# Kernel optimization log

Hardware: AMD Instinct MI355X
Metric: run time of the kernel (lower is better)

The kernel has to match this reference:

```python
import jax, jax.numpy as jnp
import numpy as np

POOLED = 7      # kernel_size
SCALE = 0.25    # spatial_scale
GMAX = 2        # upper bound of adaptive sampling grid (box sizes chosen so ceil(roi/7) <= 2)


def setup_inputs() -> dict:
    key = jax.random.key(0)
    k1, k2, k3, k4, k5, k6 = jax.random.split(key, 6)
    B, C, H, W, K = 4, 256, 128, 128, 1000
    features = jax.random.normal(k1, (B, C, H, W), dtype=jnp.float32)
    img = H / SCALE  # 512.0: image-space extent
    bidx = jax.random.randint(k2, (K,), 0, B).astype(jnp.float32)
    bw = jax.random.uniform(k3, (K,), minval=8.0, maxval=56.0)
    bh = jax.random.uniform(k4, (K,), minval=8.0, maxval=56.0)
    x1 = jax.random.uniform(k5, (K,), minval=0.0, maxval=img - 56.0)
    y1 = jax.random.uniform(k6, (K,), minval=0.0, maxval=img - 56.0)
    boxes = jnp.stack([bidx, x1, y1, x1 + bw, y1 + bh], axis=1)
    return {"features": features, "boxes": boxes}


def _sample_coords(start, bin_sz, grid):
    # start/bin_sz/grid: [K] -> coords [K, POOLED, GMAX]
    p = jnp.arange(POOLED, dtype=jnp.float32)
    i = jnp.arange(GMAX, dtype=jnp.float32)
    return (start[:, None, None] + p[None, :, None] * bin_sz[:, None, None]
            + (i[None, None, :] + 0.5) * bin_sz[:, None, None] / grid[:, None, None])


def roi_align(features, boxes):
    B, C, H, W = features.shape
    K = boxes.shape[0]
    b = boxes[:, 0].astype(jnp.int32)
    x1, y1, x2, y2 = (boxes[:, i] * SCALE for i in (1, 2, 3, 4))
    # aligned=False: no -0.5 offset, clamp roi size to >= 1
    roi_w = jnp.maximum(x2 - x1, 1.0)
    roi_h = jnp.maximum(y2 - y1, 1.0)
    bin_w = roi_w / POOLED
    bin_h = roi_h / POOLED
    # sampling_ratio = -1 -> adaptive grid = ceil(roi_size / pooled)
    gh = jnp.ceil(roi_h / POOLED)
    gw = jnp.ceil(roi_w / POOLED)

    y = _sample_coords(y1, bin_h, gh)  # [K,7,GMAX]
    x = _sample_coords(x1, bin_w, gw)  # [K,7,GMAX]
    vy = (jnp.arange(GMAX)[None, None, :] < gh[:, None, None])  # [K,1,GMAX]
    vx = (jnp.arange(GMAX)[None, None, :] < gw[:, None, None])

    # full sample grid [K, 7, GMAX, 7, GMAX] -> flatten to [K, P]
    shp = (K, POOLED, GMAX, POOLED, GMAX)
    Y = jnp.broadcast_to(y[:, :, :, None, None], shp).reshape(K, -1)
    X = jnp.broadcast_to(x[:, None, None, :, :], shp).reshape(K, -1)
    V = jnp.broadcast_to(vy[:, :, :, None, None] & vx[:, None, None, :, :], shp).reshape(K, -1)

    # bilinear interpolation, torchvision boundary semantics
    inval = (Y < -1.0) | (Y > H) | (X < -1.0) | (X > W)
    Yc = jnp.clip(Y, 0.0)
    Xc = jnp.clip(X, 0.0)
    yl = jnp.minimum(Yc.astype(jnp.int32), H - 1)
    xl = jnp.minimum(Xc.astype(jnp.int32), W - 1)
    yh = jnp.minimum(yl + 1, H - 1)
    xh = jnp.minimum(xl + 1, W - 1)
    Yc = jnp.where(yl >= H - 1, yl.astype(jnp.float32), Yc)
    Xc = jnp.where(xl >= W - 1, xl.astype(jnp.float32), Xc)
    ly = Yc - yl
    lx = Xc - xl
    hy = 1.0 - ly
    hx = 1.0 - lx
    m = jnp.where(inval | (~V), 0.0, 1.0)
    w1 = hy * hx * m; w2 = hy * lx * m; w3 = ly * hx * m; w4 = ly * lx * m

    def gather(yi, xi):
        # advanced indexing: [K,P] indices -> [K,P,C]
        return features[b[:, None], :, yi, xi]

    val = (w1[..., None] * gather(yl, xl) + w2[..., None] * gather(yl, xh)
           + w3[..., None] * gather(yh, xl) + w4[..., None] * gather(yh, xh))  # [K,P,C]
    val = val.reshape(K, POOLED, GMAX, POOLED, GMAX, C)
    out = val.sum(axis=(2, 4)) / (gh * gw)[:, None, None, None]  # [K,7,7,C]
    return jnp.transpose(out, (0, 3, 1, 2))  # [K,C,7,7]


def reference(features, boxes):
    return roi_align(features, boxes)
```

## Files before the change

### kernel.cpp

```cpp
#include <hip/hip_runtime.h>

#define POOLED 7
#define SCALE  0.25f
#define CCH    256
#define HH     128
#define WW     128
#define HW     (HH * WW)

#define NCH      16
#define NCHUNK   2
#define NBLK_PER_BOX (CCH / (NCH * NCHUNK))
#define PATCH_H  15
#define PATCH_W  16
#define PIXROW   17
#define NPIX     (14 * PIXROW + 16)
#define CHPAD    20

__global__ __launch_bounds__(256) void roi_align_kernel(
    const float* __restrict__ feat,
    const float* __restrict__ boxes,
    float* __restrict__ out,
    int K)
{
    __shared__ float patch[NPIX * CHPAD];

    int bx = blockIdx.x;
    int k  = bx >> 3;
    int cb = (bx & 7) * (NCH * NCHUNK);
    if (k >= K) return;
    int t = threadIdx.x;

    const float* box = boxes + (size_t)k * 5;
    int   b  = (int)box[0];
    float x1 = box[1] * SCALE;
    float y1 = box[2] * SCALE;
    float x2 = box[3] * SCALE;
    float y2 = box[4] * SCALE;

    float roi_w = fmaxf(x2 - x1, 1.0f);
    float roi_h = fmaxf(y2 - y1, 1.0f);
    float bin_w = roi_w * (1.0f / POOLED);
    float bin_h = roi_h * (1.0f / POOLED);
    int gw = (int)ceilf(roi_w * (1.0f / POOLED));
    int gh = (int)ceilf(roi_h * (1.0f / POOLED));
    float inv_gh = 1.0f / (float)gh;
    float inv_gw = 1.0f / (float)gw;
    int ns = gh * gw;

    float ymin = y1 + 0.5f * bin_h * inv_gh;
    float ymax = y1 + 6 * bin_h + ((gh - 1) + 0.5f) * bin_h * inv_gh;
    float xmin = x1 + 0.5f * bin_w * inv_gw;

    int ylo = min((int)fmaxf(ymin, 0.0f), HH - 1);
    int xlo = min((int)fmaxf(xmin, 0.0f), WW - 1);
    int ylmax = min((int)fmaxf(ymax, 0.0f), HH - 1);
    int h_p = min(ylmax + 1, HH - 1) - ylo + 1;
    if (h_p > PATCH_H) h_p = PATCH_H;

    int p  = t & 63;
    int pc = min(p, 48);
    int pw = pc % POOLED;
    int ph = pc / POOLED;
    int c4 = t >> 6;

    float wa[4], wb[4], wc_[4], wd[4];
    int   oa[4], ob[4], oc[4], od[4];

#pragma unroll
    for (int s = 0; s < 4; ++s) {
        if (s >= ns) break;
        int iy = s % gh;
        int ix = s / gh;

        float y = y1 + ph * bin_h + (iy + 0.5f) * bin_h * inv_gh;
        float x = x1 + pw * bin_w + (ix + 0.5f) * bin_w * inv_gw;
        bool valid = (y >= -1.0f) && (y <= (float)HH) && (x >= -1.0f) && (x <= (float)WW);

        float yc = fmaxf(y, 0.0f);
        int yl = min((int)yc, HH - 1);
        int yh2 = min(yl + 1, HH - 1);
        float ly = (yl >= HH - 1) ? 0.0f : (yc - (float)yl);
        float hy = 1.0f - ly;

        float xc = fmaxf(x, 0.0f);
        int xl = min((int)xc, WW - 1);
        int xh2 = min(xl + 1, WW - 1);
        float lx = (xl >= WW - 1) ? 0.0f : (xc - (float)xl);
        float hx = 1.0f - lx;

        float m = valid ? 1.0f : 0.0f;
        wa[s]  = hy * hx * m;
        wb[s]  = hy * lx * m;
        wc_[s] = ly * hx * m;
        wd[s]  = ly * lx * m;

        int ry  = max(0, min(yl  - ylo, h_p - 1));
        int ryh = max(0, min(yh2 - ylo, h_p - 1));
        int rxl = max(0, min(xl  - xlo, PATCH_W - 1));
        int rxh = max(0, min(xh2 - xlo, PATCH_W - 1));
        oa[s] = (ry  * PIXROW + rxl) * CHPAD;
        ob[s] = (ry  * PIXROW + rxh) * CHPAD;
        oc[s] = (ryh * PIXROW + rxl) * CHPAD;
        od[s] = (ryh * PIXROW + rxh) * CHPAD;
    }

    int lch  = t >> 4;
    int lcol = t & 15;
    int xcol = min(xlo + lcol, WW - 1);
    float sc = inv_gh * inv_gw;

    for (int ch = 0; ch < NCHUNK; ++ch) {
        if (ch) __syncthreads();

        {
            const float* g = feat + ((size_t)b * CCH + cb + ch * NCH + lch) * HW + xcol;
            float* lp = patch + lcol * CHPAD + lch;
            for (int r = 0; r < h_p; ++r) {
                lp[r * (PIXROW * CHPAD)] = g[(ylo + r) * WW];
            }
        }
        __syncthreads();

        if (p < 49) {
            float4 acc = {0.0f, 0.0f, 0.0f, 0.0f};
            const float* cp = patch + c4 * 4;
#pragma unroll
            for (int s = 0; s < 4; ++s) {
                if (s >= ns) break;
                float4 va = *(const float4*)(cp + oa[s]);
                float4 vb = *(const float4*)(cp + ob[s]);
                float4 vc = *(const float4*)(cp + oc[s]);
                float4 vd = *(const float4*)(cp + od[s]);
                float w1 = wa[s], w2 = wb[s], w3 = wc_[s], w4 = wd[s];
                acc.x += w1 * va.x + w2 * vb.x + w3 * vc.x + w4 * vd.x;
                acc.y += w1 * va.y + w2 * vb.y + w3 * vc.y + w4 * vd.y;
                acc.z += w1 * va.z + w2 * vb.z + w3 * vc.z + w4 * vd.z;
                acc.w += w1 * va.w + w2 * vb.w + w3 * vc.w + w4 * vd.w;
            }
            float* obase = out + ((size_t)k * CCH + cb + ch * NCH + c4 * 4) * 49 + p;
            obase[0]      = acc.x * sc;
            obase[49]     = acc.y * sc;
            obase[2 * 49] = acc.z * sc;
            obase[3 * 49] = acc.w * sc;
        }
    }
}

extern "C" void kernel_launch(void* const* d_in, const int* in_sizes, int n_in,
                              void* d_out, int out_size, void* d_ws, size_t ws_size,
                              hipStream_t stream) {
    const float* feat  = (const float*)d_in[0];
    const float* boxes = (const float*)d_in[1];
    float* out = (float*)d_out;

    int K = in_sizes[1] / 5;
    int blocks = K * NBLK_PER_BOX;
    roi_align_kernel<<<blocks, 256, 0, stream>>>(feat, boxes, out, K);
}
```

Baseline: 133.0 us.

## Vectorize patch loads with float4 and prefetch second channel chunk into registers

The patch load now reads float4 vectors from a 4-aligned column start, widening the patch to 20 columns, instead of scalar per-column loads in a row loop. The second channel chunk's global loads are issued before the first chunk is computed, so global latency overlaps with the LDS compute of chunk one. Sample index math swaps div/mod for shift/mask, which assumes gh is 1 or 2. This raises register use and LDS size, and the alignment clamp near the right edge needs care.

```diff
diff --git a/kernel.cpp b/kernel.cpp
--- a/kernel.cpp
+++ b/kernel.cpp
@@ -11,9 +11,10 @@
 #define NCHUNK   2
 #define NBLK_PER_BOX (CCH / (NCH * NCHUNK))
 #define PATCH_H  15
-#define PATCH_W  16
-#define PIXROW   17
-#define NPIX     (14 * PIXROW + 16)
+#define PATCH_W  20
+#define NV       5
+#define PIXROW   21
+#define NPIX     (14 * PIXROW + PATCH_W)
 #define CHPAD    20
 
 __global__ __launch_bounds__(256) void roi_align_kernel(
@@ -22,7 +23,7 @@
     float* __restrict__ out,
     int K)
 {
-    __shared__ float patch[NPIX * CHPAD];
+    __shared__ __align__(16) float patch[NPIX * CHPAD];
 
     int bx = blockIdx.x;
     int k  = bx >> 3;
@@ -53,15 +54,18 @@
 
     int ylo = min((int)fmaxf(ymin, 0.0f), HH - 1);
     int xlo = min((int)fmaxf(xmin, 0.0f), WW - 1);
+    int xlo4 = xlo & ~3;
     int ylmax = min((int)fmaxf(ymax, 0.0f), HH - 1);
     int h_p = min(ylmax + 1, HH - 1) - ylo + 1;
     if (h_p > PATCH_H) h_p = PATCH_H;
+    int mcr = min(WW - 1 - xlo4, (xlo - xlo4) + 15);
 
     int p  = t & 63;
     int pc = min(p, 48);
     int pw = pc % POOLED;
     int ph = pc / POOLED;
     int c4 = t >> 6;
+    int ghm = gh - 1;
 
     float wa[4], wb[4], wc_[4], wd[4];
     int   oa[4], ob[4], oc[4], od[4];
@@ -69,8 +73,8 @@
 #pragma unroll
     for (int s = 0; s < 4; ++s) {
         if (s >= ns) break;
-        int iy = s % gh;
-        int ix = s / gh;
+        int iy = s & ghm;
+        int ix = s >> ghm;
 
         float y = y1 + ph * bin_h + (iy + 0.5f) * bin_h * inv_gh;
         float x = x1 + pw * bin_w + (ix + 0.5f) * bin_w * inv_gw;
@@ -96,53 +100,113 @@
 
         int ry  = max(0, min(yl  - ylo, h_p - 1));
         int ryh = max(0, min(yh2 - ylo, h_p - 1));
-        int rxl = max(0, min(xl  - xlo, PATCH_W - 1));
-        int rxh = max(0, min(xh2 - xlo, PATCH_W - 1));
+        int rxl = max(0, min(xl  - xlo4, PATCH_W - 1));
+        int rxh = max(0, min(xh2 - xlo4, PATCH_W - 1));
         oa[s] = (ry  * PIXROW + rxl) * CHPAD;
         ob[s] = (ry  * PIXROW + rxh) * CHPAD;
         oc[s] = (ryh * PIXROW + rxl) * CHPAD;
         od[s] = (ryh * PIXROW + rxh) * CHPAD;
     }
 
-    int lch  = t >> 4;
-    int lcol = t & 15;
-    int xcol = min(xlo + lcol, WW - 1);
+    int lch = t >> 4;
+    int sub = t & 15;
+    int lim = h_p * NV;
+    const float* gch0 = feat + ((size_t)b * CCH + cb + lch) * HW;
+
+    bool act[NV];
+    int  goff[NV];
+    int  la[NV];
+#pragma unroll
+    for (int i = 0; i < NV; ++i) {
+        int idx = i * 16 + sub;
+        int r = idx / NV;
+        int v = idx - r * NV;
+        act[i]  = (idx < lim) && (4 * v <= mcr);
+        goff[i] = (ylo + r) * WW + min(xlo4 + 4 * v, WW - 4);
+        la[i]   = (r * PIXROW + 4 * v) * CHPAD + lch;
+    }
+
     float sc = inv_gh * inv_gw;
 
-    for (int ch = 0; ch < NCHUNK; ++ch) {
-        if (ch) __syncthreads();
-
-        {
-            const float* g = feat + ((size_t)b * CCH + cb + ch * NCH + lch) * HW + xcol;
-            float* lp = patch + lcol * CHPAD + lch;
-            for (int r = 0; r < h_p; ++r) {
-                lp[r * (PIXROW * CHPAD)] = g[(ylo + r) * WW];
-            }
-        }
-        __syncthreads();
-
-        if (p < 49) {
-            float4 acc = {0.0f, 0.0f, 0.0f, 0.0f};
-            const float* cp = patch + c4 * 4;
-#pragma unroll
-            for (int s = 0; s < 4; ++s) {
-                if (s >= ns) break;
-                float4 va = *(const float4*)(cp + oa[s]);
-                float4 vb = *(const float4*)(cp + ob[s]);
-                float4 vc = *(const float4*)(cp + oc[s]);
-                float4 vd = *(const float4*)(cp + od[s]);
-                float w1 = wa[s], w2 = wb[s], w3 = wc_[s], w4 = wd[s];
-                acc.x += w1 * va.x + w2 * vb.x + w3 * vc.x + w4 * vd.x;
-                acc.y += w1 * va.y + w2 * vb.y + w3 * vc.y + w4 * vd.y;
-                acc.z += w1 * va.z + w2 * vb.z + w3 * vc.z + w4 * vd.z;
-                acc.w += w1 * va.w + w2 * vb.w + w3 * vc.w + w4 * vd.w;
-            }
-            float* obase = out + ((size_t)k * CCH + cb + ch * NCH + c4 * 4) * 49 + p;
-            obase[0]      = acc.x * sc;
-            obase[49]     = acc.y * sc;
-            obase[2 * 49] = acc.z * sc;
-            obase[3 * 49] = acc.w * sc;
-        }
+    float4 v0[NV];
+#pragma unroll
+    for (int i = 0; i < NV; ++i)
+        if (act[i]) v0[i] = *(const float4*)(gch0 + goff[i]);
+#pragma unroll
+    for (int i = 0; i < NV; ++i)
+        if (act[i]) {
+            float* lp = patch + la[i];
+            lp[0]         = v0[i].x;
+            lp[CHPAD]     = v0[i].y;
+            lp[2 * CHPAD] = v0[i].z;
+            lp[3 * CHPAD] = v0[i].w;
+        }
+
+    const float* gch1 = gch0 + (size_t)NCH * HW;
+    float4 v1[NV];
+#pragma unroll
+    for (int i = 0; i < NV; ++i)
+        if (act[i]) v1[i] = *(const float4*)(gch1 + goff[i]);
+
+    __syncthreads();
+
+    if (p < 49) {
+        float4 acc = {0.0f, 0.0f, 0.0f, 0.0f};
+        const float* cp = patch + c4 * 4;
+#pragma unroll
+        for (int s = 0; s < 4; ++s) {
+            if (s >= ns) break;
+            float4 va = *(const float4*)(cp + oa[s]);
+            float4 vb = *(const float4*)(cp + ob[s]);
+            float4 vc = *(const float4*)(cp + oc[s]);
+            float4 vd = *(const float4*)(cp + od[s]);
+            float w1 = wa[s], w2 = wb[s], w3 = wc_[s], w4 = wd[s];
+            acc.x += w1 * va.x + w2 * vb.x + w3 * vc.x + w4 * vd.x;
+            acc.y += w1 * va.y + w2 * vb.y + w3 * vc.y + w4 * vd.y;
+            acc.z += w1 * va.z + w2 * vb.z + w3 * vc.z + w4 * vd.z;
+            acc.w += w1 * va.w + w2 * vb.w + w3 * vc.w + w4 * vd.w;
+        }
+        float* obase = out + ((size_t)k * CCH + cb + c4 * 4) * 49 + p;
+        obase[0]      = acc.x * sc;
+        obase[49]     = acc.y * sc;
+        obase[2 * 49] = acc.z * sc;
+        obase[3 * 49] = acc.w * sc;
+    }
+
+    __syncthreads();
+
+#pragma unroll
+    for (int i = 0; i < NV; ++i)
+        if (act[i]) {
+            float* lp = patch + la[i];
+            lp[0]         = v1[i].x;
+            lp[CHPAD]     = v1[i].y;
+            lp[2 * CHPAD] = v1[i].z;
+            lp[3 * CHPAD] = v1[i].w;
+        }
+    __syncthreads();
+
+    if (p < 49) {
+        float4 acc = {0.0f, 0.0f, 0.0f, 0.0f};
+        const float* cp = patch + c4 * 4;
+#pragma unroll
+        for (int s = 0; s < 4; ++s) {
+            if (s >= ns) break;
+            float4 va = *(const float4*)(cp + oa[s]);
+            float4 vb = *(const float4*)(cp + ob[s]);
+            float4 vc = *(const float4*)(cp + oc[s]);
+            float4 vd = *(const float4*)(cp + od[s]);
+            float w1 = wa[s], w2 = wb[s], w3 = wc_[s], w4 = wd[s];
+            acc.x += w1 * va.x + w2 * vb.x + w3 * vc.x + w4 * vd.x;
+            acc.y += w1 * va.y + w2 * vb.y + w3 * vc.y + w4 * vd.y;
+            acc.z += w1 * va.z + w2 * vb.z + w3 * vc.z + w4 * vd.z;
+            acc.w += w1 * va.w + w2 * vb.w + w3 * vc.w + w4 * vd.w;
+        }
+        float* obase = out + ((size_t)k * CCH + cb + NCH + c4 * 4) * 49 + p;
+        obase[0]      = acc.x * sc;
+        obase[49]     = acc.y * sc;
+        obase[2 * 49] = acc.z * sc;
+        obase[3 * 49] = acc.w * sc;
     }
 }
 
```

New measurement: 127.2 us. -4.3%, faster.

## Vectorize patch loads as float4 and prefetch second channel chunk

Applied to the files above, without the earlier changes.

Patch loading switches from one scalar global load per row per thread to aligned float4 loads over a 4-aligned column window. The window is widened to 19 columns so each row is covered by five vector loads. The second channel chunk is issued into registers before the first chunk is computed, which overlaps its global latency with the first bilinear pass. Sample weights are built from separable per-axis terms with uniform scalars, and launch bounds ask for 7 blocks per CU. The cost is higher register pressure, larger shared memory, and more complex indexing near the right image edge.

```diff
diff --git a/kernel.cpp b/kernel.cpp
--- a/kernel.cpp
+++ b/kernel.cpp
@@ -11,18 +11,19 @@
 #define NCHUNK   2
 #define NBLK_PER_BOX (CCH / (NCH * NCHUNK))
 #define PATCH_H  15
-#define PATCH_W  16
-#define PIXROW   17
-#define NPIX     (14 * PIXROW + 16)
+#define NV       5
+#define PIXROW   19
+#define NPIX     (PATCH_H * PIXROW)
 #define CHPAD    20
-
-__global__ __launch_bounds__(256) void roi_align_kernel(
+#define ROWSTR   (PIXROW * CHPAD)
+
+__global__ __launch_bounds__(256, 7) void roi_align_kernel(
     const float* __restrict__ feat,
     const float* __restrict__ boxes,
     float* __restrict__ out,
     int K)
 {
-    __shared__ float patch[NPIX * CHPAD];
+    __shared__ __align__(16) float patch[NPIX * CHPAD];
 
     int bx = blockIdx.x;
     int k  = bx >> 3;
@@ -30,7 +31,7 @@
     if (k >= K) return;
     int t = threadIdx.x;
 
-    const float* box = boxes + (size_t)k * 5;
+    const float* box = boxes + k * 5;
     int   b  = (int)box[0];
     float x1 = box[1] * SCALE;
     float y1 = box[2] * SCALE;
@@ -45,7 +46,6 @@
     int gh = (int)ceilf(roi_h * (1.0f / POOLED));
     float inv_gh = 1.0f / (float)gh;
     float inv_gw = 1.0f / (float)gw;
-    int ns = gh * gw;
 
     float ymin = y1 + 0.5f * bin_h * inv_gh;
     float ymax = y1 + 6 * bin_h + ((gh - 1) + 0.5f) * bin_h * inv_gh;
@@ -53,97 +53,173 @@
 
     int ylo = min((int)fmaxf(ymin, 0.0f), HH - 1);
     int xlo = min((int)fmaxf(xmin, 0.0f), WW - 1);
+    int xlo4 = xlo & ~3;
     int ylmax = min((int)fmaxf(ymax, 0.0f), HH - 1);
     int h_p = min(ylmax + 1, HH - 1) - ylo + 1;
     if (h_p > PATCH_H) h_p = PATCH_H;
+    int mcr = min(WW - 1 - xlo4, (xlo - xlo4) + 14);
+
+    int s_b   = __builtin_amdgcn_readfirstlane(b);
+    int s_ylo = __builtin_amdgcn_readfirstlane(ylo);
+    int s_x4  = __builtin_amdgcn_readfirstlane(xlo4);
+    int s_hp  = __builtin_amdgcn_readfirstlane(h_p);
+    int s_mcr = __builtin_amdgcn_readfirstlane(mcr);
+    int s_ns  = __builtin_amdgcn_readfirstlane(gh * gw);
+    int ghm   = __builtin_amdgcn_readfirstlane(gh - 1);
 
     int p  = t & 63;
     int pc = min(p, 48);
     int pw = pc % POOLED;
     int ph = pc / POOLED;
-    int c4 = t >> 6;
+    int cg = t >> 6;
+
+    float yb = y1 + ph * bin_h;
+    float xb = x1 + pw * bin_w;
+
+    float hy0, ly0, hy1, ly1;
+    int   ryT0, ryhT0, ryT1, ryhT1;
+    float hx0, lx0, hx1, lx1;
+    int   rxT0, rxhT0, rxT1, rxhT1;
+
+#define YSIDE(IYC, HY, LY, RT, RHT) {                                   \
+        float y = yb + IYC * bin_h * inv_gh;                            \
+        bool vld = (y >= -1.0f) && (y <= (float)HH);                    \
+        float yc = fmaxf(y, 0.0f);                                      \
+        int yl = min((int)yc, HH - 1);                                  \
+        int yh2 = min(yl + 1, HH - 1);                                  \
+        float ly = (yl >= HH - 1) ? 0.0f : (yc - (float)yl);            \
+        HY = vld ? (1.0f - ly) : 0.0f;                                  \
+        LY = vld ? ly : 0.0f;                                           \
+        int ry  = max(0, min(yl  - s_ylo, s_hp - 1));                   \
+        int ryh = max(0, min(yh2 - s_ylo, s_hp - 1));                   \
+        RT  = ry  * ROWSTR;                                             \
+        RHT = ryh * ROWSTR;                                             \
+    }
+#define XSIDE(IXC, HX, LX, RT, RHT) {                                   \
+        float x = xb + IXC * bin_w * inv_gw;                            \
+        bool vld = (x >= -1.0f) && (x <= (float)WW);                    \
+        float xc = fmaxf(x, 0.0f);                                      \
+        int xl = min((int)xc, WW - 1);                                  \
+        int xh2 = min(xl + 1, WW - 1);                                  \
+        float lx = (xl >= WW - 1) ? 0.0f : (xc - (float)xl);            \
+        HX = vld ? (1.0f - lx) : 0.0f;                                  \
+        LX = vld ? lx : 0.0f;                                           \
+        int rxl = max(0, min(xl  - s_x4, PIXROW - 1));                  \
+        int rxh = max(0, min(xh2 - s_x4, PIXROW - 1));                  \
+        RT  = rxl * CHPAD;                                              \
+        RHT = rxh * CHPAD;                                              \
+    }
+    YSIDE(0.5f, hy0, ly0, ryT0, ryhT0)
+    YSIDE(1.5f, hy1, ly1, ryT1, ryhT1)
+    XSIDE(0.5f, hx0, lx0, rxT0, rxhT0)
+    XSIDE(1.5f, hx1, lx1, rxT1, rxhT1)
+#undef YSIDE
+#undef XSIDE
 
     float wa[4], wb[4], wc_[4], wd[4];
     int   oa[4], ob[4], oc[4], od[4];
-
-#pragma unroll
-    for (int s = 0; s < 4; ++s) {
-        if (s >= ns) break;
-        int iy = s % gh;
-        int ix = s / gh;
-
-        float y = y1 + ph * bin_h + (iy + 0.5f) * bin_h * inv_gh;
-        float x = x1 + pw * bin_w + (ix + 0.5f) * bin_w * inv_gw;
-        bool valid = (y >= -1.0f) && (y <= (float)HH) && (x >= -1.0f) && (x <= (float)WW);
-
-        float yc = fmaxf(y, 0.0f);
-        int yl = min((int)yc, HH - 1);
-        int yh2 = min(yl + 1, HH - 1);
-        float ly = (yl >= HH - 1) ? 0.0f : (yc - (float)yl);
-        float hy = 1.0f - ly;
-
-        float xc = fmaxf(x, 0.0f);
-        int xl = min((int)xc, WW - 1);
-        int xh2 = min(xl + 1, WW - 1);
-        float lx = (xl >= WW - 1) ? 0.0f : (xc - (float)xl);
-        float hx = 1.0f - lx;
-
-        float m = valid ? 1.0f : 0.0f;
-        wa[s]  = hy * hx * m;
-        wb[s]  = hy * lx * m;
-        wc_[s] = ly * hx * m;
-        wd[s]  = ly * lx * m;
-
-        int ry  = max(0, min(yl  - ylo, h_p - 1));
-        int ryh = max(0, min(yh2 - ylo, h_p - 1));
-        int rxl = max(0, min(xl  - xlo, PATCH_W - 1));
-        int rxh = max(0, min(xh2 - xlo, PATCH_W - 1));
-        oa[s] = (ry  * PIXROW + rxl) * CHPAD;
-        ob[s] = (ry  * PIXROW + rxh) * CHPAD;
-        oc[s] = (ryh * PIXROW + rxl) * CHPAD;
-        od[s] = (ryh * PIXROW + rxh) * CHPAD;
-    }
-
-    int lch  = t >> 4;
-    int lcol = t & 15;
-    int xcol = min(xlo + lcol, WW - 1);
+    wa[0] = hy0 * hx0; wb[0] = hy0 * lx0; wc_[0] = ly0 * hx0; wd[0] = ly0 * lx0;
+    oa[0] = ryT0 + rxT0;  ob[0] = ryT0 + rxhT0;
+    oc[0] = ryhT0 + rxT0; od[0] = ryhT0 + rxhT0;
+    {
+        float hyS = ghm ? hy1 : hy0, lyS = ghm ? ly1 : ly0;
+        int ryS = ghm ? ryT1 : ryT0, ryhS = ghm ? ryhT1 : ryhT0;
+        float hxS = ghm ? hx0 : hx1, lxS = ghm ? lx0 : lx1;
+        int rxS = ghm ? rxT0 : rxT1, rxhS = ghm ? rxhT0 : rxhT1;
+        wa[1] = hyS * hxS; wb[1] = hyS * lxS; wc_[1] = lyS * hxS; wd[1] = lyS * lxS;
+        oa[1] = ryS + rxS;  ob[1] = ryS + rxhS;
+        oc[1] = ryhS + rxS; od[1] = ryhS + rxhS;
+    }
+    wa[2] = hy0 * hx1; wb[2] = hy0 * lx1; wc_[2] = ly0 * hx1; wd[2] = ly0 * lx1;
+    oa[2] = ryT0 + rxT1;  ob[2] = ryT0 + rxhT1;
+    oc[2] = ryhT0 + rxT1; od[2] = ryhT0 + rxhT1;
+    wa[3] = hy1 * hx1; wb[3] = hy1 * lx1; wc_[3] = ly1 * hx1; wd[3] = ly1 * lx1;
+    oa[3] = ryT1 + rxT1;  ob[3] = ryT1 + rxhT1;
+    oc[3] = ryhT1 + rxT1; od[3] = ryhT1 + rxhT1;
+
+    int lch = t >> 4;
+    int sub = t & 15;
+    int lim = s_hp * NV;
+    const float* gch0 = feat + (s_b * CCH + cb + lch) * HW;
+
+    bool act[NV], actw[NV];
+    int  goff[NV];
+    int  la[NV];
+#pragma unroll
+    for (int i = 0; i < NV; ++i) {
+        int idx = i * 16 + sub;
+        int r = idx / NV;
+        int v = idx - r * NV;
+        act[i]  = (idx < lim) && (4 * v <= s_mcr);
+        actw[i] = act[i] && (v < 4);
+        goff[i] = (s_ylo + r) * WW + min(s_x4 + 4 * v, WW - 4);
+        la[i]   = (r * PIXROW + 4 * v) * CHPAD + lch;
+    }
+
     float sc = inv_gh * inv_gw;
 
-    for (int ch = 0; ch < NCHUNK; ++ch) {
-        if (ch) __syncthreads();
-
-        {
-            const float* g = feat + ((size_t)b * CCH + cb + ch * NCH + lch) * HW + xcol;
-            float* lp = patch + lcol * CHPAD + lch;
-            for (int r = 0; r < h_p; ++r) {
-                lp[r * (PIXROW * CHPAD)] = g[(ylo + r) * WW];
-            }
+    float4 u0[NV];
+#pragma unroll
+    for (int i = 0; i < NV; ++i)
+        if (act[i]) u0[i] = *(const float4*)(gch0 + goff[i]);
+#pragma unroll
+    for (int i = 0; i < NV; ++i)
+        if (act[i]) {
+            float* lp = patch + la[i];
+            lp[0]         = u0[i].x;
+            lp[CHPAD]     = u0[i].y;
+            lp[2 * CHPAD] = u0[i].z;
+            if (actw[i]) lp[3 * CHPAD] = u0[i].w;
         }
-        __syncthreads();
-
-        if (p < 49) {
-            float4 acc = {0.0f, 0.0f, 0.0f, 0.0f};
-            const float* cp = patch + c4 * 4;
-#pragma unroll
-            for (int s = 0; s < 4; ++s) {
-                if (s >= ns) break;
-                float4 va = *(const float4*)(cp + oa[s]);
-                float4 vb = *(const float4*)(cp + ob[s]);
-                float4 vc = *(const float4*)(cp + oc[s]);
-                float4 vd = *(const float4*)(cp + od[s]);
-                float w1 = wa[s], w2 = wb[s], w3 = wc_[s], w4 = wd[s];
-                acc.x += w1 * va.x + w2 * vb.x + w3 * vc.x + w4 * vd.x;
-                acc.y += w1 * va.y + w2 * vb.y + w3 * vc.y + w4 * vd.y;
-                acc.z += w1 * va.z + w2 * vb.z + w3 * vc.z + w4 * vd.z;
-                acc.w += w1 * va.w + w2 * vb.w + w3 * vc.w + w4 * vd.w;
-            }
-            float* obase = out + ((size_t)k * CCH + cb + ch * NCH + c4 * 4) * 49 + p;
-            obase[0]      = acc.x * sc;
-            obase[49]     = acc.y * sc;
-            obase[2 * 49] = acc.z * sc;
-            obase[3 * 49] = acc.w * sc;
+
+    const float* gch1 = gch0 + NCH * HW;
+    float4 u1[NV];
+#pragma unroll
+    for (int i = 0; i < NV; ++i)
+        if (act[i]) u1[i] = *(const float4*)(gch1 + goff[i]);
+
+    __syncthreads();
+
+#define BILIN(S) {                                                      \
+        float4 va = *(const float4*)(cp + oa[S]);                       \
+        float4 vb = *(const float4*)(cp + ob[S]);                       \
+        float4 vc = *(const float4*)(cp + oc[S]);                       \
+        float4 vd = *(const float4*)(cp + od[S]);                       \
+        float w1 = wa[S], w2 = wb[S], w3 = wc_[S], w4 = wd[S];          \
+        acc.x += w1 * va.x + w2 * vb.x + w3 * vc.x + w4 * vd.x;         \
+        acc.y += w1 * va.y + w2 * vb.y + w3 * vc.y + w4 * vd.y;         \
+        acc.z += w1 * va.z + w2 * vb.z + w3 * vc.z + w4 * vd.z;         \
+        acc.w += w1 * va.w + w2 * vb.w + w3 * vc.w + w4 * vd.w;         \
+    }
+#define COMPUTE(CHB) {                                                  \
+        float4 acc = {0.0f, 0.0f, 0.0f, 0.0f};                          \
+        const float* cp = patch + cg * 4;                               \
+        BILIN(0)                                                        \
+        if (s_ns > 1) BILIN(1)                                          \
+        if (s_ns > 2) { BILIN(2) BILIN(3) }                             \
+        int ob_ = (k * CCH + cb + (CHB) + cg * 4) * 49 + p;             \
+        out[ob_]          = acc.x * sc;                                 \
+        out[ob_ + 49]     = acc.y * sc;                                 \
+        out[ob_ + 2 * 49] = acc.z * sc;                                 \
+        out[ob_ + 3 * 49] = acc.w * sc;                                 \
+    }
+
+    if (p < 49) COMPUTE(0)
+
+    __syncthreads();
+
+#pragma unroll
+    for (int i = 0; i < NV; ++i)
+        if (act[i]) {
+            float* lp = patch + la[i];
+            lp[0]         = u1[i].x;
+            lp[CHPAD]     = u1[i].y;
+            lp[2 * CHPAD] = u1[i].z;
+            if (actw[i]) lp[3 * CHPAD] = u1[i].w;
         }
-    }
+    __syncthreads();
+
+    if (p < 49) COMPUTE(NCH)
 }
 
 extern "C" void kernel_launch(void* const* d_in, const int* in_sizes, int n_in,
```

Result: slower. 193.7 us (+45.7%).
